# Optimization experiments

Measured on AMD Instinct MI355X. Metric: run time of the kernel, lower is better.

## Reference

```python
import jax, jax.numpy as jnp
import numpy as np

N_GRAPHS = 2048
BN_EPS = 1e-5


def _lin_init(k, fan_in, fan_out):
    kw, kb = jax.random.split(k)
    s = 1.0 / np.sqrt(fan_in)
    w = jax.random.uniform(kw, (fan_in, fan_out), minval=-s, maxval=s, dtype=jnp.float32)
    b = jax.random.uniform(kb, (fan_out,), minval=-s, maxval=s, dtype=jnp.float32)
    return w, b


def setup_inputs() -> dict:
    key = jax.random.key(0)
    ks = jax.random.split(key, 16)
    N, E, F, H, C = 100000, 600000, 7, 128, 2
    inp = {}
    inp["x"] = jax.random.normal(ks[0], (N, F), dtype=jnp.float32)
    inp["edge_index"] = jax.random.randint(ks[1], (2, E), 0, N)
    inp["edge_attr"] = jax.random.normal(ks[2], (E,), dtype=jnp.float32)  # ignored by GINConv
    inp["batch"] = jnp.sort(jax.random.randint(ks[3], (N,), 0, N_GRAPHS))
    # GINConv inner MLPs: [in, H, H]
    inp["g1_w1"], inp["g1_b1"] = _lin_init(ks[4], F, H)
    inp["g1_w2"], inp["g1_b2"] = _lin_init(ks[5], H, H)
    inp["g2_w1"], inp["g2_b1"] = _lin_init(ks[6], H, H)
    inp["g2_w2"], inp["g2_b2"] = _lin_init(ks[7], H, H)
    inp["g3_w1"], inp["g3_b1"] = _lin_init(ks[8], H, H)
    inp["g3_w2"], inp["g3_b2"] = _lin_init(ks[9], H, H)
    # JumpingKnowledge('cat') projection: 3H -> H
    inp["jk_w"], inp["jk_b"] = _lin_init(ks[10], 3 * H, H)
    # classifier MLP [H, H, C] with batch_norm on hidden layer
    inp["c1_w"], inp["c1_b"] = _lin_init(ks[11], H, H)
    inp["bn_g"] = jnp.ones((H,), jnp.float32)
    inp["bn_b"] = jnp.zeros((H,), jnp.float32)
    inp["c2_w"], inp["c2_b"] = _lin_init(ks[12], H, C)
    return inp


def reference(x, edge_index, edge_attr, batch,
              g1_w1, g1_b1, g1_w2, g1_b2,
              g2_w1, g2_b1, g2_w2, g2_b2,
              g3_w1, g3_b1, g3_w2, g3_b2,
              jk_w, jk_b, c1_w, c1_b, bn_g, bn_b, c2_w, c2_b):
    src, dst = edge_index[0], edge_index[1]
    N = x.shape[0]

    def gin_conv(h, w1, b1, w2, b2):
        # sum aggregation of neighbor messages; eps=0 -> (1+eps)*x + aggr = x + aggr
        agg = jax.ops.segment_sum(h[src], dst, num_segments=N)
        z = h + agg
        return jax.nn.relu(z @ w1 + b1) @ w2 + b2  # inner MLP, plain last layer

    # BasicGNN applies act (ReLU) after each conv; dropout=eval (identity)
    h1 = jax.nn.relu(gin_conv(x, g1_w1, g1_b1, g1_w2, g1_b2))
    h2 = jax.nn.relu(gin_conv(h1, g2_w1, g2_b1, g2_w2, g2_b2))
    h3 = jax.nn.relu(gin_conv(h2, g3_w1, g3_b1, g3_w2, g3_b2))

    h = jnp.concatenate([h1, h2, h3], axis=-1) @ jk_w + jk_b  # jk='cat' + final lin
    g = jax.ops.segment_sum(h, batch, num_segments=N_GRAPHS)  # global_add_pool -> [G, H]

    z = g @ c1_w + c1_b
    mu = z.mean(axis=0)
    var = z.var(axis=0)
    z = (z - mu) * jax.lax.rsqrt(var + BN_EPS) * bn_g + bn_b  # batch_norm (batch stats)
    z = jax.nn.relu(z)
    return z @ c2_w + c2_b  # [G, num_classes]
```

## Files before the change

### kernel.cpp

```cpp
#include <hip/hip_runtime.h>

#define NGRAPH 2048
#define EIDX_CAP 1024

typedef __attribute__((ext_vector_type(4))) float f32x4;
typedef __attribute__((ext_vector_type(8))) _Float16 h16x8;
typedef __attribute__((ext_vector_type(2))) _Float16 h16x2;

__global__ __launch_bounds__(256) void scan_onepass(
    const int* __restrict__ deg, int* __restrict__ rowstart, int* __restrict__ cursor,
    unsigned* __restrict__ scanst, int N, int E, int nchunk)
{
  __shared__ int tmp[256];
  __shared__ int sh_chunk;
  __shared__ int sh_exc;
  int tid = threadIdx.x;
  if (tid == 0) sh_chunk = (int)atomicAdd(&scanst[nchunk], 1u);
  __syncthreads();
  int cb = sh_chunk;
  int i = cb * 256 + tid;
  int v = (i < N) ? deg[i] : 0;
  tmp[tid] = v;
  __syncthreads();
#pragma unroll
  for (int off = 1; off < 256; off <<= 1) {
    int t = (tid >= off) ? tmp[tid - off] : 0;
    __syncthreads();
    tmp[tid] += t;
    __syncthreads();
  }
  int aggregate = tmp[255];
  const unsigned VMASK = (1u << 30) - 1u;

  if (cb == 0) {
    if (tid == 0) {
      atomicExch(&scanst[0], (2u << 30) | (unsigned)aggregate);
      sh_exc = 0;
    }
  } else {
    if (tid < 64) {
      if (tid == 0) atomicExch(&scanst[cb], (1u << 30) | (unsigned)aggregate);
      int excv = 0;
      int base = cb - 1;
      for (;;) {
        int j = base - tid;
        unsigned s = 0u;
        if (j >= 0) {
          do { s = atomicAdd(&scanst[j], 0u); } while ((s >> 30) == 0u);
        }
        unsigned long long pm = __ballot(j >= 0 && (s >> 30) == 2u);
        if (pm) {
          int pl = __ffsll((long long)pm) - 1;
          if (tid <= pl && j >= 0) excv += (int)(s & VMASK);
          break;
        }
        if (j >= 0) excv += (int)(s & VMASK);
        base -= 64;
        if (base < 0) break;
      }
#pragma unroll
      for (int off = 32; off > 0; off >>= 1) excv += __shfl_xor(excv, off, 64);
      if (tid == 0) {
        sh_exc = excv;
        atomicExch(&scanst[cb], (2u << 30) | (unsigned)(excv + aggregate));
      }
    }
  }
  __syncthreads();
  int exc = sh_exc;
  if (i < N) {
    int rs = exc + tmp[tid] - v;
    rowstart[i] = rs;
    cursor[i] = rs;
  }
  if (cb == nchunk - 1 && tid == 0) rowstart[N] = E;
}

__global__ __launch_bounds__(256) void fill_eidx(
    const int* __restrict__ src, const int* __restrict__ dst,
    int* __restrict__ cursor, int* __restrict__ eidx, int E)
{
  int e = blockIdx.x * 256 + threadIdx.x;
  if (e >= E) return;
  int d = dst[e];
  int pos = atomicAdd(&cursor[d], 1);
  eidx[pos] = src[e];
}

struct WPs {
  const float* w[5];
  _Float16* hi[5];
  _Float16* lo[5];
};
__global__ __launch_bounds__(256) void prep_hist(
    WPs p, const float* __restrict__ x, _Float16* __restrict__ x8h, int N,
    const int* __restrict__ dst, int* __restrict__ deg, int E,
    const int* __restrict__ batch, int* __restrict__ gstart,
    float* __restrict__ bnstat,
    const float* __restrict__ jkw, const float* __restrict__ jkb,
    const float* __restrict__ c1w, float* __restrict__ wc, float* __restrict__ bcv)
{
  int g = blockIdx.x * 256 + threadIdx.x;
  if (g < E) {
    atomicAdd(&deg[dst[g]], 1);
    return;
  }
  int q = g - E;
  if (q < 5 * 16384) {
    int m = q >> 14;
    int j = q & 16383;
    int c = j >> 3, e = j & 7;
    int t = c >> 8, kc = (c >> 6) & 3, lane = c & 63;
    int n = t * 16 + (lane & 15);
    int k = kc * 32 + (lane >> 4) * 8 + e;
    float w = p.w[m][k * 128 + n];
    _Float16 h = (_Float16)w;
    p.hi[m][j] = h;
    p.lo[m][j] = (_Float16)(w - (float)h);
    return;
  }
  q -= 5 * 16384;
  if (q < N * 8) {
    int v = q >> 3, j = q & 7;
    x8h[q] = (_Float16)((j < 7) ? x[(long)v * 7 + j] : 0.f);
    return;
  }
  q -= N * 8;
  if (q < 256) { bnstat[q] = 0.f; return; }
  q -= 256;
  if (q < N) {
    int b = batch[q];
    int bp = (q > 0) ? batch[q - 1] : -1;
    for (int gg = bp + 1; gg <= b; ++gg) gstart[gg] = q;
    if (q == N - 1)
      for (int gg = b + 1; gg <= NGRAPH; ++gg) gstart[gg] = N;
    return;
  }
  q -= N;
  if (q < 384 * 128) {
    int k = q >> 7, n = q & 127;
    float acc = 0.f;
#pragma unroll 8
    for (int h = 0; h < 128; ++h)
      acc += jkw[k * 128 + h] * c1w[h * 128 + n];
    wc[q] = acc;
    return;
  }
  q -= 384 * 128;
  if (q < 128) {
    float acc = 0.f;
#pragma unroll 8
    for (int h = 0; h < 128; ++h)
      acc += jkb[h] * c1w[h * 128 + q];
    bcv[q] = acc;
  }
}

__device__ inline void mfma_pass(
    const _Float16* __restrict__ zbuf,
    const _Float16* __restrict__ Whi, const _Float16* __restrict__ Wlo,
    int rw, int m16, int quad, int lane, f32x4 acc[8])
{
  int r = rw + m16;
  const _Float16* zrow = &zbuf[r * 128];
#pragma unroll
  for (int kc = 0; kc < 4; ++kc) {
    int cidx = kc * 4 + quad;
    h16x8 ah = *(const h16x8*)&zrow[((cidx + r) & 15) * 8];
#pragma unroll
    for (int t = 0; t < 8; ++t) {
      long cb = ((t * 4 + kc) * 64 + lane) * 8;
      h16x8 bh = *(const h16x8*)&Whi[cb];
      h16x8 bl = *(const h16x8*)&Wlo[cb];
      acc[t] = __builtin_amdgcn_mfma_f32_16x16x32_f16(ah, bh, acc[t], 0, 0, 0);
      acc[t] = __builtin_amdgcn_mfma_f32_16x16x32_f16(ah, bl, acc[t], 0, 0, 0);
    }
  }
}

__global__ __launch_bounds__(256, 5) void fused_gin(
    const _Float16* __restrict__ H, const int* __restrict__ rowstart,
    const int* __restrict__ eidx,
    const _Float16* __restrict__ W1hi, const _Float16* __restrict__ W1lo,
    const float* __restrict__ B1,
    const _Float16* __restrict__ W2hi, const _Float16* __restrict__ W2lo,
    const float* __restrict__ B2,
    _Float16* __restrict__ Out, int M)
{
  __shared__ _Float16 zbuf[64 * 128];
  __shared__ int sh_rs[65];
  __shared__ int sh_ei[EIDX_CAP];
  int tid = threadIdx.x;
  int rbase = blockIdx.x * 64;

  if (tid < 65) {
    int v = rbase + tid;
    sh_rs[tid] = rowstart[(v < M) ? v : M];
  }
  __syncthreads();
  int e_begin = sh_rs[0];
  int cnt = sh_rs[64] - e_begin;
  if (cnt <= EIDX_CAP) {
    for (int i = tid; i < cnt; i += 256) sh_ei[i] = eidx[e_begin + i];
  }
  __syncthreads();

  {
    int sub = tid & 15;
    int ng = tid >> 4;
    const _Float16* Hc = H + sub * 8;
    if (cnt <= EIDX_CAP) {
#pragma unroll 1
      for (int it = 0; it < 4; ++it) {
        int r = it * 16 + ng;
        int v = rbase + r;
        int vc = (v < M) ? v : (M - 1);
        h16x8 sv = *(const h16x8*)&Hc[(long)vc * 128];
        float a0[8], a1[8];
#pragma unroll
        for (int j = 0; j < 8; ++j) { a0[j] = (float)sv[j]; a1[j] = 0.f; }
        int e = sh_rs[r] - e_begin;
        int e1 = sh_rs[r + 1] - e_begin;
#pragma unroll 1
        for (; e < e1; e += 8) {
          int last = e1 - 1;
          int s0 = sh_ei[e];
          int s1 = sh_ei[(e + 1 < e1) ? e + 1 : last];
          int s2 = sh_ei[(e + 2 < e1) ? e + 2 : last];
          int s3 = sh_ei[(e + 3 < e1) ? e + 3 : last];
          int s4 = sh_ei[(e + 4 < e1) ? e + 4 : last];
          int s5 = sh_ei[(e + 5 < e1) ? e + 5 : last];
          int s6 = sh_ei[(e + 6 < e1) ? e + 6 : last];
          int s7 = sh_ei[(e + 7 < e1) ? e + 7 : last];
          float m1 = (e + 1 < e1) ? 1.f : 0.f;
          float m2 = (e + 2 < e1) ? 1.f : 0.f;
          float m3 = (e + 3 < e1) ? 1.f : 0.f;
          float m4 = (e + 4 < e1) ? 1.f : 0.f;
          float m5 = (e + 5 < e1) ? 1.f : 0.f;
          float m6 = (e + 6 < e1) ? 1.f : 0.f;
          float m7 = (e + 7 < e1) ? 1.f : 0.f;
          h16x8 h0 = *(const h16x8*)&Hc[(long)s0 * 128];
          h16x8 h1 = *(const h16x8*)&Hc[(long)s1 * 128];
          h16x8 h2 = *(const h16x8*)&Hc[(long)s2 * 128];
          h16x8 h3 = *(const h16x8*)&Hc[(long)s3 * 128];
          h16x8 h4 = *(const h16x8*)&Hc[(long)s4 * 128];
          h16x8 h5 = *(const h16x8*)&Hc[(long)s5 * 128];
          h16x8 h6 = *(const h16x8*)&Hc[(long)s6 * 128];
          h16x8 h7 = *(const h16x8*)&Hc[(long)s7 * 128];
#pragma unroll
          for (int j = 0; j < 8; ++j) {
            a0[j] += (float)h0[j] + m2 * (float)h2[j] + m4 * (float)h4[j] + m6 * (float)h6[j];
            a1[j] += m1 * (float)h1[j] + m3 * (float)h3[j] + m5 * (float)h5[j] + m7 * (float)h7[j];
          }
        }
        h16x8 zo;
#pragma unroll
        for (int j = 0; j < 8; ++j) zo[j] = (_Float16)(a0[j] + a1[j]);
        *(h16x8*)&zbuf[r * 128 + ((sub + r) & 15) * 8] = zo;
      }
    } else {
#pragma unroll 1
      for (int it = 0; it < 4; ++it) {
        int r = it * 16 + ng;
        int v = rbase + r;
        int vc = (v < M) ? v : (M - 1);
        h16x8 sv = *(const h16x8*)&Hc[(long)vc * 128];
        float a0[8], a1[8];
#pragma unroll
        for (int j = 0; j < 8; ++j) { a0[j] = (float)sv[j]; a1[j] = 0.f; }
        int e = sh_rs[r], e1 = sh_rs[r + 1];
        for (; e + 2 <= e1; e += 2) {
          int s0 = eidx[e], s1 = eidx[e + 1];
          h16x8 h0 = *(const h16x8*)&Hc[(long)s0 * 128];
          h16x8 h1 = *(const h16x8*)&Hc[(long)s1 * 128];
#pragma unroll
          for (int j = 0; j < 8; ++j) { a0[j] += (float)h0[j]; a1[j] += (float)h1[j]; }
        }
        if (e < e1) {
          int s = eidx[e];
          h16x8 h = *(const h16x8*)&Hc[(long)s * 128];
#pragma unroll
          for (int j = 0; j < 8; ++j) a1[j] += (float)h[j];
        }
        h16x8 zo;
#pragma unroll
        for (int j = 0; j < 8; ++j) zo[j] = (_Float16)(a0[j] + a1[j]);
        *(h16x8*)&zbuf[r * 128 + ((sub + r) & 15) * 8] = zo;
      }
    }
  }
  __syncthreads();

  int lane = tid & 63;
  int wv = tid >> 6;
  int m16 = lane & 15;
  int quad = lane >> 4;
  int rw = wv * 16;

  f32x4 acc[8];
#pragma unroll
  for (int t = 0; t < 8; ++t) acc[t] = (f32x4){0.f, 0.f, 0.f, 0.f};
  mfma_pass(zbuf, W1hi, W1lo, rw, m16, quad, lane, acc);

  float bias[8];
#pragma unroll
  for (int t = 0; t < 8; ++t) bias[t] = B1[t * 16 + m16];

#pragma unroll
  for (int i = 0; i < 4; ++i) {
    int r = rw + quad * 4 + i;
#pragma unroll
    for (int t = 0; t < 8; ++t) {
      int col = t * 16 + m16;
      int cidx = col >> 3;
      zbuf[r * 128 + ((cidx + r) & 15) * 8 + (col & 7)] =
          (_Float16)fmaxf(acc[t][i] + bias[t], 0.f);
    }
  }

#pragma unroll
  for (int t = 0; t < 8; ++t) acc[t] = (f32x4){0.f, 0.f, 0.f, 0.f};
  mfma_pass(zbuf, W2hi, W2lo, rw, m16, quad, lane, acc);

#pragma unroll
  for (int t = 0; t < 8; ++t) bias[t] = B2[t * 16 + m16];

#pragma unroll
  for (int i = 0; i < 4; ++i) {
    int r = rw + quad * 4 + i;
#pragma unroll
    for (int t = 0; t < 8; ++t) {
      int col = t * 16 + m16;
      int cidx = col >> 3;
      zbuf[r * 128 + ((cidx + r) & 15) * 8 + (col & 7)] =
          (_Float16)fmaxf(acc[t][i] + bias[t], 0.f);
    }
  }
  {
    int rr2 = tid >> 2, c4 = tid & 3;
    int r = rbase + rr2;
    if (r < M) {
#pragma unroll
      for (int it = 0; it < 4; ++it) {
        int cidx = it * 4 + c4;
        h16x8 vv = *(const h16x8*)&zbuf[rr2 * 128 + ((cidx + rr2) & 15) * 8];
        *(h16x8*)&Out[(long)r * 128 + cidx * 8] = vv;
      }
    }
  }
}

__global__ __launch_bounds__(256, 8) void fused_l1(
    const _Float16* __restrict__ x8h, const int* __restrict__ rowstart,
    const int* __restrict__ eidx,
    const float* __restrict__ W1, const float* __restrict__ B1,
    const _Float16* __restrict__ W2hi, const _Float16* __restrict__ W2lo,
    const float* __restrict__ B2, _Float16* __restrict__ Out, int M)
{
  __shared__ _Float16 ybuf[64 * 128];
  __shared__ float z1s[64][8];
  int tid = threadIdx.x;
  int rbase = blockIdx.x * 64;

  {
    int node = tid >> 2, sub = tid & 3;
    int v = rbase + node;
    int vc = (v < M) ? v : (M - 1);
    float a[8];
    if (sub == 0) {
      h16x8 sv = *(const h16x8*)&x8h[(long)vc * 8];
#pragma unroll
      for (int j = 0; j < 8; ++j) a[j] = (float)sv[j];
    } else {
#pragma unroll
      for (int j = 0; j < 8; ++j) a[j] = 0.f;
    }
    int e0 = rowstart[vc], e1 = rowstart[vc + 1];
    int e = e0 + sub;
    for (; e + 4 < e1; e += 8) {
      int s0 = eidx[e], s1 = eidx[e + 4];
      h16x8 h0 = *(const h16x8*)&x8h[(long)s0 * 8];
      h16x8 h1 = *(const h16x8*)&x8h[(long)s1 * 8];
#pragma unroll
      for (int j = 0; j < 8; ++j) a[j] += (float)h0[j] + (float)h1[j];
    }
    if (e < e1) {
      int s = eidx[e];
      h16x8 h = *(const h16x8*)&x8h[(long)s * 8];
#pragma unroll
      for (int j = 0; j < 8; ++j) a[j] += (float)h[j];
    }
#pragma unroll
    for (int j = 0; j < 8; ++j) {
      a[j] += __shfl_xor(a[j], 1, 64);
      a[j] += __shfl_xor(a[j], 2, 64);
    }
    if (sub == 0) {
#pragma unroll
      for (int j = 0; j < 8; ++j) z1s[node][j] = a[j];
    }
  }
  __syncthreads();

  {
    int c = tid & 127;
    int cidx = c >> 3, celt = c & 7;
    int rh0 = (tid >> 7) * 32;
    float w1r[7];
#pragma unroll
    for (int k = 0; k < 7; ++k) w1r[k] = W1[k * 128 + c];
    float b1 = B1[c];
#pragma unroll 4
    for (int rr = 0; rr < 32; ++rr) {
      int r = rh0 + rr;
      const float* zp = z1s[r];
      float a = b1;
#pragma unroll
      for (int k = 0; k < 7; ++k) a += zp[k] * w1r[k];
      ybuf[r * 128 + ((cidx + r) & 15) * 8 + celt] = (_Float16)fmaxf(a, 0.f);
    }
  }
  __syncthreads();

  int lane = tid & 63;
  int wv = tid >> 6;
  int m16 = lane & 15;
  int quad = lane >> 4;
  int rw = wv * 16;

  f32x4 acc[8];
#pragma unroll
  for (int t = 0; t < 8; ++t) acc[t] = (f32x4){0.f, 0.f, 0.f, 0.f};
  mfma_pass(ybuf, W2hi, W2lo, rw, m16, quad, lane, acc);

  float bias[8];
#pragma unroll
  for (int t = 0; t < 8; ++t) bias[t] = B2[t * 16 + m16];

#pragma unroll
  for (int i = 0; i < 4; ++i) {
    int r = rw + quad * 4 + i;
#pragma unroll
    for (int t = 0; t < 8; ++t) {
      int col = t * 16 + m16;
      int cidx = col >> 3;
      ybuf[r * 128 + ((cidx + r) & 15) * 8 + (col & 7)] =
          (_Float16)fmaxf(acc[t][i] + bias[t], 0.f);
    }
  }
  {
    int rr2 = tid >> 2, c4 = tid & 3;
    int r = rbase + rr2;
    if (r < M) {
#pragma unroll
      for (int it = 0; it < 4; ++it) {
        int cidx = it * 4 + c4;
        h16x8 vv = *(const h16x8*)&ybuf[rr2 * 128 + ((cidx + rr2) & 15) * 8];
        *(h16x8*)&Out[(long)r * 128 + cidx * 8] = vv;
      }
    }
  }
}

__global__ __launch_bounds__(256) void pool_direct(
    const _Float16* __restrict__ H1, const _Float16* __restrict__ H2,
    const _Float16* __restrict__ H3, const int* __restrict__ gstart,
    float* __restrict__ P)
{
  __shared__ float red[3 * 16 * 8 * 4];
  int g = blockIdx.x;
  int s = gstart[g], e = gstart[g + 1];
  int tid = threadIdx.x;
  int wv = tid >> 6, lane = tid & 63;
  int tbl = lane >> 4;
  int ch = lane & 15;
  float a[8];
#pragma unroll
  for (int j = 0; j < 8; ++j) a[j] = 0.f;
  if (tbl < 3) {
    const _Float16* A = (tbl == 0) ? H1 : ((tbl == 1) ? H2 : H3);
    const _Float16* Ac = A + ch * 8;
    for (int r = s + wv; r < e; r += 4) {
      h16x8 v = *(const h16x8*)&Ac[(long)r * 128];
#pragma unroll
      for (int j = 0; j < 8; ++j) a[j] += (float)v[j];
    }
#pragma unroll
    for (int j = 0; j < 8; ++j) red[((tbl * 16 + ch) * 8 + j) * 4 + wv] = a[j];
  }
  __syncthreads();
  for (int t = tid; t < 384; t += 256) {
    float4 rv = *(const float4*)&red[t * 4];
    P[(long)g * 384 + t] = rv.x + rv.y + rv.z + rv.w;
  }
}

__global__ __launch_bounds__(256) void jk_bn(
    const float* __restrict__ P, const int* __restrict__ gstart,
    const float* __restrict__ Wc, const float* __restrict__ bc,
    const float* __restrict__ c1b,
    float* __restrict__ zc, float* __restrict__ bnstat)
{
  __shared__ float pl[8 * 384];
  __shared__ float red[512];
  int tid = threadIdx.x, blk = blockIdx.x;
  int r0 = blk * 8;
  for (int o = tid; o < 8 * 384; o += 256)
    pl[o] = P[(long)r0 * 384 + o];
  __syncthreads();
  int col = tid & 127, rg = tid >> 7;
  float acc[4];
  float b0 = bc[col], b1 = c1b[col];
#pragma unroll
  for (int i = 0; i < 4; ++i) {
    int row = r0 + rg + 2 * i;
    float cntv = (float)(gstart[row + 1] - gstart[row]);
    acc[i] = cntv * b0 + b1;
  }
#pragma unroll 4
  for (int k = 0; k < 384; ++k) {
    float w = Wc[k * 128 + col];
#pragma unroll
    for (int i = 0; i < 4; ++i)
      acc[i] += pl[(rg + 2 * i) * 384 + k] * w;
  }
  float s = 0.f, s2 = 0.f;
#pragma unroll
  for (int i = 0; i < 4; ++i) {
    int row = r0 + rg + 2 * i;
    zc[(long)row * 128 + col] = acc[i];
    s += acc[i]; s2 += acc[i] * acc[i];
  }
  red[tid] = s; red[256 + tid] = s2;
  __syncthreads();
  if (tid < 128) {
    atomicAdd(&bnstat[tid], red[tid] + red[tid + 128]);
    atomicAdd(&bnstat[128 + tid], red[256 + tid] + red[256 + tid + 128]);
  }
}

__global__ __launch_bounds__(256) void bn_final(
    const float* __restrict__ ZC, const float* __restrict__ bnstat,
    const float* __restrict__ gma, const float* __restrict__ bta,
    const float* __restrict__ W2, const float* __restrict__ B2, float* __restrict__ out)
{
  __shared__ float scl[128], shf[128];
  __shared__ float zl[64 * 132];
  int tid = threadIdx.x;
  if (tid < 128) {
    float mu = bnstat[tid] * (1.f / NGRAPH);
    float var = bnstat[128 + tid] * (1.f / NGRAPH) - mu * mu;
    float rs = rsqrtf(var + 1e-5f);
    float sc = gma[tid] * rs;
    scl[tid] = sc;
    shf[tid] = bta[tid] - mu * sc;
  }
  int g0 = blockIdx.x * 64;
  for (int i = tid; i < 64 * 128; i += 256) {
    int r = i >> 7, c = i & 127;
    zl[r * 132 + c] = ZC[(long)(g0 + r) * 128 + c];
  }
  __syncthreads();
  int q = tid >> 2, sub = tid & 3;
  int g = g0 + q;
  float a0 = 0.f, a1 = 0.f;
#pragma unroll 8
  for (int hh = 0; hh < 32; ++hh) {
    int h = sub + hh * 4;
    float zn = zl[q * 132 + h] * scl[h] + shf[h];
    zn = fmaxf(zn, 0.f);
    a0 += zn * W2[2 * h];
    a1 += zn * W2[2 * h + 1];
  }
  a0 += __shfl_xor(a0, 1, 64); a0 += __shfl_xor(a0, 2, 64);
  a1 += __shfl_xor(a1, 1, 64); a1 += __shfl_xor(a1, 2, 64);
  if (sub == 0) {
    out[2 * g] = a0 + B2[0];
    out[2 * g + 1] = a1 + B2[1];
  }
}

extern "C" void kernel_launch(void* const* d_in, const int* in_sizes, int n_in,
                              void* d_out, int out_size, void* d_ws, size_t ws_size,
                              hipStream_t stream)
{
  const float* x    = (const float*)d_in[0];
  const int*   ei   = (const int*)d_in[1];
  const int*   batch = (const int*)d_in[3];
  const float* g1w1 = (const float*)d_in[4];  const float* g1b1 = (const float*)d_in[5];
  const float* g1w2 = (const float*)d_in[6];  const float* g1b2 = (const float*)d_in[7];
  const float* g2w1 = (const float*)d_in[8];  const float* g2b1 = (const float*)d_in[9];
  const float* g2w2 = (const float*)d_in[10]; const float* g2b2 = (const float*)d_in[11];
  const float* g3w1 = (const float*)d_in[12]; const float* g3b1 = (const float*)d_in[13];
  const float* g3w2 = (const float*)d_in[14]; const float* g3b2 = (const float*)d_in[15];
  const float* jkw  = (const float*)d_in[16]; const float* jkb  = (const float*)d_in[17];
  const float* c1w  = (const float*)d_in[18]; const float* c1b  = (const float*)d_in[19];
  const float* bng  = (const float*)d_in[20]; const float* bnb  = (const float*)d_in[21];
  const float* c2w  = (const float*)d_in[22]; const float* c2b  = (const float*)d_in[23];

  const int N = in_sizes[3];
  const int E = in_sizes[1] / 2;
  const int* src = ei;
  const int* dst = ei + E;

  char* w = (char*)d_ws;
  auto alloc = [&](size_t bytes) {
    char* p = w;
    w += (bytes + 255) & ~(size_t)255;
    return p;
  };
  _Float16* hA = (_Float16*)alloc((size_t)N * 128 * 2);
  _Float16* hB = (_Float16*)alloc((size_t)N * 128 * 2);
  _Float16* hC = (_Float16*)alloc((size_t)N * 128 * 2);
  _Float16* x8h = (_Float16*)alloc((size_t)N * 8 * 2);
  float* P       = (float*)alloc((size_t)NGRAPH * 384 * 4);
  float* bnstat  = (float*)alloc(256 * 4);
  float* zc   = (float*)alloc((size_t)NGRAPH * 128 * 4);
  float* wc   = (float*)alloc((size_t)384 * 128 * 4);
  float* bcv  = (float*)alloc((size_t)128 * 4);
  int* deg      = (int*)alloc((size_t)N * 4);
  unsigned* scanst = (unsigned*)alloc((size_t)1024 * 4);
  int* cursor   = (int*)alloc((size_t)N * 4);
  int* rowstart = (int*)alloc((size_t)(N + 1) * 4);
  int* eidx     = (int*)alloc((size_t)E * 4);
  int* gstart   = (int*)alloc((size_t)(NGRAPH + 1) * 4);
  _Float16* wtbuf = (_Float16*)alloc((size_t)5 * 2 * 16384 * 2);

  _Float16* WThi[5];
  _Float16* WTlo[5];
  for (int m = 0; m < 5; ++m) {
    WThi[m] = wtbuf + (size_t)m * 2 * 16384;
    WTlo[m] = WThi[m] + 16384;
  }

  const int nchunk = (N + 255) / 256;
  const int eb = (E + 255) / 256;

  hipMemsetAsync(deg, 0, (size_t)((char*)(scanst + 1024) - (char*)deg), stream);

  {
    WPs p;
    p.w[0] = g1w2; p.w[1] = g2w1; p.w[2] = g2w2; p.w[3] = g3w1; p.w[4] = g3w2;
    for (int m = 0; m < 5; ++m) { p.hi[m] = WThi[m]; p.lo[m] = WTlo[m]; }
    int total = E + 5 * 16384 + N * 8 + 256 + N + 384 * 128 + 128;
    prep_hist<<<(total + 255) / 256, 256, 0, stream>>>(p, x, x8h, N, dst, deg, E,
                                                       batch, gstart, bnstat,
                                                       jkw, jkb, c1w, wc, bcv);
  }

  scan_onepass<<<nchunk, 256, 0, stream>>>(deg, rowstart, cursor, scanst, N, E, nchunk);
  fill_eidx<<<eb, 256, 0, stream>>>(src, dst, cursor, eidx, E);

  const int fBlocks = (N + 63) / 64;

  fused_l1<<<fBlocks, 256, 0, stream>>>(x8h, rowstart, eidx, g1w1, g1b1,
      WThi[0], WTlo[0], g1b2, hC, N);
  fused_gin<<<fBlocks, 256, 0, stream>>>(hC, rowstart, eidx,
      WThi[1], WTlo[1], g2b1, WThi[2], WTlo[2], g2b2, hB, N);
  fused_gin<<<fBlocks, 256, 0, stream>>>(hB, rowstart, eidx,
      WThi[3], WTlo[3], g3b1, WThi[4], WTlo[4], g3b2, hA, N);

  pool_direct<<<NGRAPH, 256, 0, stream>>>(hC, hB, hA, gstart, P);

  jk_bn<<<NGRAPH / 8, 256, 0, stream>>>(P, gstart, wc, bcv, c1b, zc, bnstat);
  bn_final<<<NGRAPH / 64, 256, 0, stream>>>(zc, bnstat, bng, bnb, c2w, c2b, (float*)d_out);
}
```

Measured before the change: 389.0 us.

## Fuse degree histogram, scan and CSR fill into one persistent kernel

Merges the degree histogram (formerly inside prep_hist), the one-pass scan and the eidx fill into a single build_csr kernel of nchunk blocks. The phases are separated by software grid barriers built on atomic counters in scanst. This removes two kernel launches and the dependency gaps between them. It relies on all 391 blocks being resident at once; if they are not, the spin barrier deadlocks. It also drops the dynamic chunk ordering, and the scan lookback now depends on blockIdx order.

After: 481.6 us. 1.24x slower.

```diff
diff --git a/kernel.cpp b/kernel.cpp
--- a/kernel.cpp
+++ b/kernel.cpp
@@ -7,17 +7,29 @@
 typedef __attribute__((ext_vector_type(8))) _Float16 h16x8;
 typedef __attribute__((ext_vector_type(2))) _Float16 h16x2;
 
-__global__ __launch_bounds__(256) void scan_onepass(
-    const int* __restrict__ deg, int* __restrict__ rowstart, int* __restrict__ cursor,
-    unsigned* __restrict__ scanst, int N, int E, int nchunk)
+__global__ __launch_bounds__(256) void build_csr(
+    const int* __restrict__ src, const int* __restrict__ dst,
+    int* __restrict__ deg, int* __restrict__ rowstart, int* __restrict__ cursor,
+    int* __restrict__ eidx, unsigned* __restrict__ scanst, int N, int E, int nchunk)
 {
   __shared__ int tmp[256];
-  __shared__ int sh_chunk;
   __shared__ int sh_exc;
   int tid = threadIdx.x;
-  if (tid == 0) sh_chunk = (int)atomicAdd(&scanst[nchunk], 1u);
-  __syncthreads();
-  int cb = sh_chunk;
+  int cb = blockIdx.x;
+  int gsz = nchunk * 256;
+
+  for (int e = cb * 256 + tid; e < E; e += gsz)
+    atomicAdd(&deg[dst[e]], 1);
+
+  __threadfence();
+  __syncthreads();
+  if (tid == 0) {
+    atomicAdd(&scanst[1000], 1u);
+    while (atomicAdd(&scanst[1000], 0u) < (unsigned)nchunk)
+      __builtin_amdgcn_s_sleep(8);
+  }
+  __syncthreads();
+
   int i = cb * 256 + tid;
   int v = (i < N) ? deg[i] : 0;
   tmp[tid] = v;
@@ -74,17 +86,21 @@
     cursor[i] = rs;
   }
   if (cb == nchunk - 1 && tid == 0) rowstart[N] = E;
-}
-
-__global__ __launch_bounds__(256) void fill_eidx(
-    const int* __restrict__ src, const int* __restrict__ dst,
-    int* __restrict__ cursor, int* __restrict__ eidx, int E)
-{
-  int e = blockIdx.x * 256 + threadIdx.x;
-  if (e >= E) return;
-  int d = dst[e];
-  int pos = atomicAdd(&cursor[d], 1);
-  eidx[pos] = src[e];
+
+  __threadfence();
+  __syncthreads();
+  if (tid == 0) {
+    atomicAdd(&scanst[1001], 1u);
+    while (atomicAdd(&scanst[1001], 0u) < (unsigned)nchunk)
+      __builtin_amdgcn_s_sleep(8);
+  }
+  __syncthreads();
+
+  for (int e = cb * 256 + tid; e < E; e += gsz) {
+    int d = dst[e];
+    int pos = atomicAdd(&cursor[d], 1);
+    eidx[pos] = src[e];
+  }
 }
 
 struct WPs {
@@ -94,18 +110,12 @@
 };
 __global__ __launch_bounds__(256) void prep_hist(
     WPs p, const float* __restrict__ x, _Float16* __restrict__ x8h, int N,
-    const int* __restrict__ dst, int* __restrict__ deg, int E,
     const int* __restrict__ batch, int* __restrict__ gstart,
     float* __restrict__ bnstat,
     const float* __restrict__ jkw, const float* __restrict__ jkb,
     const float* __restrict__ c1w, float* __restrict__ wc, float* __restrict__ bcv)
 {
-  int g = blockIdx.x * 256 + threadIdx.x;
-  if (g < E) {
-    atomicAdd(&deg[dst[g]], 1);
-    return;
-  }
-  int q = g - E;
+  int q = blockIdx.x * 256 + threadIdx.x;
   if (q < 5 * 16384) {
     int m = q >> 14;
     int j = q & 16383;
@@ -634,22 +644,21 @@
   }
 
   const int nchunk = (N + 255) / 256;
-  const int eb = (E + 255) / 256;
 
   hipMemsetAsync(deg, 0, (size_t)((char*)(scanst + 1024) - (char*)deg), stream);
+
+  build_csr<<<nchunk, 256, 0, stream>>>(src, dst, deg, rowstart, cursor, eidx,
+                                        scanst, N, E, nchunk);
 
   {
     WPs p;
     p.w[0] = g1w2; p.w[1] = g2w1; p.w[2] = g2w2; p.w[3] = g3w1; p.w[4] = g3w2;
     for (int m = 0; m < 5; ++m) { p.hi[m] = WThi[m]; p.lo[m] = WTlo[m]; }
-    int total = E + 5 * 16384 + N * 8 + 256 + N + 384 * 128 + 128;
-    prep_hist<<<(total + 255) / 256, 256, 0, stream>>>(p, x, x8h, N, dst, deg, E,
+    int total = 5 * 16384 + N * 8 + 256 + N + 384 * 128 + 128;
+    prep_hist<<<(total + 255) / 256, 256, 0, stream>>>(p, x, x8h, N,
                                                        batch, gstart, bnstat,
                                                        jkw, jkb, c1w, wc, bcv);
   }
-
-  scan_onepass<<<nchunk, 256, 0, stream>>>(deg, rowstart, cursor, scanst, N, E, nchunk);
-  fill_eidx<<<eb, 256, 0, stream>>>(src, dst, cursor, eidx, E);
 
   const int fBlocks = (N + 63) / 64;
 
```
